# Kernel tuning notes

Hardware: AMD Instinct MI355X
Metric: run time of the kernel (lower is better)

## Reference

```python
import jax, jax.numpy as jnp
import numpy as np

B, S, D, H = 8, 1024, 1024, 16
DH = D // H


def setup_inputs() -> dict:
    key = jax.random.key(0)
    ks = jax.random.split(key, 11)
    sc = 0.02
    inp = {"inputs": jax.random.normal(ks[0], (B, S, D), dtype=jnp.float32)}
    for i, name in enumerate(["q", "k", "v", "r", "o"]):
        inp[f"W{name}"] = jax.random.normal(ks[1 + 2 * i], (D, D), dtype=jnp.float32) * sc
        inp[f"b{name}"] = jax.random.normal(ks[2 + 2 * i], (D,), dtype=jnp.float32) * sc
    return inp


def _heads(x):
    # [B, S, D] -> [B, H, S, DH]
    b, s, d = x.shape
    return x.reshape(b, s, H, DH).transpose(0, 2, 1, 3)


def reference(inputs, Wq, bq, Wk, bk, Wv, bv, Wr, br, Wo, bo):
    q = inputs @ Wq.T + bq
    k = inputs @ Wk.T + bk
    v = inputs @ Wv.T + bv
    r = inputs @ Wr.T + br
    qh, kh, vh = _heads(q), _heads(k), _heads(v)
    scores = jnp.einsum("bhsd,bhtd->bhst", qh, kh) / jnp.sqrt(jnp.float32(DH))
    attn = jax.nn.softmax(scores, axis=-1)
    # custom value transform: softmax(QK^T) @ log(sigmoid(V)), then exp
    y = jnp.exp(jnp.einsum("bhst,bhtd->bhsd", attn, jax.nn.log_sigmoid(vh)))
    # [B, H, S, DH] -> [B, S, D]
    y = y.transpose(0, 2, 1, 3).reshape(inputs.shape)
    y = r * y  # gated
    y = y @ Wo.T + bo
    return y + inputs
```

## Files before the change

kernel.cpp:

```cpp
#include <hip/hip_runtime.h>
#include <math.h>

#define Bq   8
#define Sq   1024
#define Dq   1024
#define Hq   16
#define DHq  64
#define Mq   (Bq*Sq)

typedef unsigned short u16;
typedef unsigned int   u32;
typedef __attribute__((ext_vector_type(4))) float  f4;
typedef __attribute__((ext_vector_type(4))) u16    u16x4;
typedef __attribute__((ext_vector_type(8))) __bf16 bf16x8;
typedef __attribute__((ext_vector_type(4))) float  f32x4;

#define MFMA16(acc, a, b) __builtin_amdgcn_mfma_f32_16x16x32_bf16(a, b, acc, 0, 0, 0)

__device__ __forceinline__ u16 f2b(float f) {
  u32 u = __float_as_uint(f);
  u32 r = u + 0x7FFFu + ((u >> 16) & 1u);
  return (u16)(r >> 16);
}
__device__ __forceinline__ float b2f(u16 h) {
  return __uint_as_float(((u32)h) << 16);
}
__device__ __forceinline__ float logsig(float x) {
  return fminf(x, 0.f) - log1pf(__expf(-fabsf(x)));
}
__device__ __forceinline__ void gld16(const u16* g, u16* l) {
  __builtin_amdgcn_global_load_lds(
      (const __attribute__((address_space(1))) void*)g,
      (__attribute__((address_space(3))) void*)l, 16, 0, 0);
}

__global__ __launch_bounds__(256) void cvt_kernel(const float* __restrict__ s,
                                                  u16* __restrict__ d, int n4) {
  int i = blockIdx.x * 256 + threadIdx.x;
  if (i >= n4) return;
  f4 v = *(const f4*)(s + 4 * (size_t)i);
  u32 p0 = (u32)f2b(v[0]) | ((u32)f2b(v[1]) << 16);
  u32 p1 = (u32)f2b(v[2]) | ((u32)f2b(v[3]) << 16);
  u32* dp = (u32*)(d + 4 * (size_t)i);
  dp[0] = p0; dp[1] = p1;
}

__device__ __forceinline__ void gemm_body(
    u16* As, u16* Ws_, const u16* __restrict__ A, const u16* __restrict__ W,
    const float* __restrict__ bias, const float* __restrict__ resid,
    u16* __restrict__ ob, float* __restrict__ of, int mode)
{
  char* Asc = (char*)As;
  char* Wsc = (char*)Ws_;
  const int tid = threadIdx.x;
  const int l  = tid & 63, w = tid >> 6;
  const int lo = l & 15,  lg = l >> 4;
  const int m0 = blockIdx.x * 128;
  const int n0 = blockIdx.y * 128;
  const int wr = (w >> 1) * 64;
  const int wc = (w & 1) * 64;
  const int srow = tid >> 3;
  const int scbs = ((tid & 7) * 16) ^ ((srow & 7) << 4);
  const u16* Ag = A + (size_t)(m0 + srow) * Dq + (scbs >> 1);
  const u16* Wg = W + (size_t)(n0 + srow) * Dq + (scbs >> 1);
  u16* Ad = As  + tid * 8;
  u16* Wd = Ws_ + tid * 8;

  f32x4 acc[4][4];
  #pragma unroll
  for (int i = 0; i < 4; ++i)
    #pragma unroll
    for (int j = 0; j < 4; ++j) acc[i][j] = (f32x4){0.f, 0.f, 0.f, 0.f};

  for (int k0 = 0; k0 < Dq; k0 += 64) {
    __syncthreads();
    #pragma unroll
    for (int t = 0; t < 4; ++t) {
      gld16(Ag + (size_t)t * 32 * Dq + k0, Ad + t * 32 * 64);
      gld16(Wg + (size_t)t * 32 * Dq + k0, Wd + t * 32 * 64);
    }
    __syncthreads();

    #pragma unroll
    for (int kc = 0; kc < 2; ++kc) {
      bf16x8 af[4], bfr[4];
      #pragma unroll
      for (int ff = 0; ff < 4; ++ff) {
        int ra = wr + ff * 16 + lo;
        int rb = wc + ff * 16 + lo;
        int cb = kc * 64 + lg * 16;
        af[ff]  = *(const bf16x8*)(Asc + ra * 128 + (cb ^ ((ra & 7) << 4)));
        bfr[ff] = *(const bf16x8*)(Wsc + rb * 128 + (cb ^ ((rb & 7) << 4)));
      }
      #pragma unroll
      for (int mf = 0; mf < 4; ++mf)
        #pragma unroll
        for (int nf = 0; nf < 4; ++nf)
          acc[mf][nf] = MFMA16(acc[mf][nf], af[mf], bfr[nf]);
    }
  }

  #pragma unroll
  for (int nf = 0; nf < 4; ++nf) {
    const int n = n0 + wc + nf * 16 + lo;
    const float bn = bias[n];
    if (mode == 2) {
      const int hidx = n >> 6, dh = n & 63;
      #pragma unroll
      for (int mf = 0; mf < 4; ++mf) {
        const int m = m0 + wr + mf * 16 + lg * 4;
        const int bidx = m >> 10, s = m & 1023;
        u16x4 pk;
        #pragma unroll
        for (int r = 0; r < 4; ++r) pk[r] = f2b(logsig(acc[mf][nf][r] + bn));
        *(u16x4*)(ob + ((size_t)(bidx * Hq + hidx) * DHq + dh) * Sq + s) = pk;
      }
    } else {
      #pragma unroll
      for (int mf = 0; mf < 4; ++mf) {
        #pragma unroll
        for (int r = 0; r < 4; ++r) {
          const int m = m0 + wr + mf * 16 + lg * 4 + r;
          float y = acc[mf][nf][r] + bn;
          if (mode == 0) {
            size_t a = ((size_t)((m >> 10) * Hq + (n >> 6)) * Sq + (m & 1023)) * DHq + (n & 63);
            ob[a] = f2b(y * 0.125f);
          } else if (mode == 1) {
            size_t a = ((size_t)((m >> 10) * Hq + (n >> 6)) * Sq + (m & 1023)) * DHq + (n & 63);
            ob[a] = f2b(y);
          } else if (mode == 3) {
            ob[(size_t)m * Dq + n] = f2b(y);
          } else {
            of[(size_t)m * Dq + n] = y + resid[(size_t)m * Dq + n];
          }
        }
      }
    }
  }
}

__global__ __launch_bounds__(256) void proj_kernel(
    const u16* __restrict__ Xb,
    const u16* __restrict__ Wq, const float* __restrict__ bq, u16* qh,
    const u16* __restrict__ Wk, const float* __restrict__ bk, u16* kh,
    const u16* __restrict__ Wv, const float* __restrict__ bv, u16* lsvt,
    const u16* __restrict__ Wr, const float* __restrict__ br, u16* rh)
{
  __shared__ u16 As[128 * 64];
  __shared__ u16 Ws_[128 * 64];
  const u16* W; const float* bb; u16* o; int mode = blockIdx.z;
  switch (blockIdx.z) {
    case 0:  W = Wq; bb = bq; o = qh;   break;
    case 1:  W = Wk; bb = bk; o = kh;   break;
    case 2:  W = Wv; bb = bv; o = lsvt; break;
    default: W = Wr; bb = br; o = rh;   break;
  }
  gemm_body(As, Ws_, Xb, W, bb, nullptr, o, nullptr, mode);
}

__global__ __launch_bounds__(256) void out_kernel(
    const u16* __restrict__ G, const u16* __restrict__ Wo,
    const float* __restrict__ bo, const float* __restrict__ X,
    float* __restrict__ out)
{
  __shared__ u16 As[128 * 64];
  __shared__ u16 Ws_[128 * 64];
  gemm_body(As, Ws_, G, Wo, bo, X, nullptr, out, 4);
}

__global__ __launch_bounds__(256) void attn_kernel(
    const u16* __restrict__ qh, const u16* __restrict__ kh,
    const u16* __restrict__ lsvt, const u16* __restrict__ rh,
    u16* __restrict__ g)
{
  __shared__ u16 Ks[2][64 * 64];
  __shared__ u16 Ls[2][64 * 64];
  __shared__ u16 Ps[128 * 64];
  char* Pc = (char*)Ps;

  const int tid = threadIdx.x;
  const int l  = tid & 63, w = tid >> 6;
  const int lo = l & 15,  lg = l >> 4;
  const int s0 = blockIdx.x * 128;
  const int h = blockIdx.y, b = blockIdx.z;
  const size_t hb = (size_t)(b * Hq + h) * (Sq * DHq);
  const int srow = tid >> 3;
  const int scbs = ((tid & 7) * 16) ^ ((srow & 7) << 4);

  bf16x8 qf[2][2];
  #pragma unroll
  for (int i = 0; i < 2; ++i)
    #pragma unroll
    for (int kc = 0; kc < 2; ++kc)
      qf[i][kc] = *(const bf16x8*)(qh + hb +
                    (size_t)(s0 + w * 32 + i * 16 + lo) * DHq + kc * 32 + lg * 8);

  float l_lane[2][4];
  f32x4 oacc[2][4];
  #pragma unroll
  for (int i = 0; i < 2; ++i)
    #pragma unroll
    for (int rr = 0; rr < 4; ++rr) l_lane[i][rr] = 0.f;
  #pragma unroll
  for (int i = 0; i < 2; ++i)
    #pragma unroll
    for (int f = 0; f < 4; ++f) oacc[i][f] = (f32x4){0.f, 0.f, 0.f, 0.f};

  auto stage = [&](int kt, int bb) {
    const u16* kg = kh   + hb + (size_t)(kt * 64 + srow) * DHq + (scbs >> 1);
    const u16* lg_ = lsvt + hb + (size_t)srow * Sq + kt * 64 + (scbs >> 1);
    u16* kd = (u16*)Ks[bb] + tid * 8;
    u16* ld = (u16*)Ls[bb] + tid * 8;
    gld16(kg, kd);
    gld16(kg + (size_t)32 * DHq, kd + 32 * 64);
    gld16(lg_, ld);
    gld16(lg_ + (size_t)32 * Sq, ld + 32 * 64);
  };

  stage(0, 0);
  for (int kt = 0; kt < 16; ++kt) {
    const int cur = kt & 1;
    __syncthreads();
    if (kt < 15) stage(kt + 1, cur ^ 1);
    char* Kc = (char*)Ks[cur];
    char* Lc = (char*)Ls[cur];

    f32x4 sf[2][4];
    #pragma unroll
    for (int f = 0; f < 4; ++f) {
      int rk = f * 16 + lo;
      int sw = (rk & 7) << 4;
      bf16x8 k0 = *(const bf16x8*)(Kc + rk * 128 + ((lg * 16) ^ sw));
      bf16x8 k1 = *(const bf16x8*)(Kc + rk * 128 + ((64 + lg * 16) ^ sw));
      #pragma unroll
      for (int i = 0; i < 2; ++i) {
        f32x4 s = (f32x4){0.f, 0.f, 0.f, 0.f};
        s = MFMA16(s, qf[i][0], k0);
        s = MFMA16(s, qf[i][1], k1);
        sf[i][f] = s;
      }
    }

    #pragma unroll
    for (int i = 0; i < 2; ++i) {
      const int prbase = w * 32 + i * 16 + lg * 4;
      #pragma unroll
      for (int rr = 0; rr < 4; ++rr) {
        float p0 = __expf(sf[i][0][rr]);
        float p1 = __expf(sf[i][1][rr]);
        float p2 = __expf(sf[i][2][rr]);
        float p3 = __expf(sf[i][3][rr]);
        l_lane[i][rr] += (p0 + p1) + (p2 + p3);
        const int pr = prbase + rr;
        const int sw = (pr & 7) << 4;
        *(u16*)(Pc + pr * 128 + ((lo * 2 +  0) ^ sw)) = f2b(p0);
        *(u16*)(Pc + pr * 128 + ((lo * 2 + 32) ^ sw)) = f2b(p1);
        *(u16*)(Pc + pr * 128 + ((lo * 2 + 64) ^ sw)) = f2b(p2);
        *(u16*)(Pc + pr * 128 + ((lo * 2 + 96) ^ sw)) = f2b(p3);
      }
    }
    __syncthreads();

    bf16x8 pa[2][2];
    #pragma unroll
    for (int i = 0; i < 2; ++i) {
      const int pr = w * 32 + i * 16 + lo;
      const int psw = (pr & 7) << 4;
      pa[i][0] = *(const bf16x8*)(Pc + pr * 128 + ((lg * 16) ^ psw));
      pa[i][1] = *(const bf16x8*)(Pc + pr * 128 + ((64 + lg * 16) ^ psw));
    }
    #pragma unroll
    for (int dhf = 0; dhf < 4; ++dhf) {
      const int rl = dhf * 16 + lo;
      const int lsw = (rl & 7) << 4;
      bf16x8 l0 = *(const bf16x8*)(Lc + rl * 128 + ((lg * 16) ^ lsw));
      bf16x8 l1 = *(const bf16x8*)(Lc + rl * 128 + ((64 + lg * 16) ^ lsw));
      #pragma unroll
      for (int i = 0; i < 2; ++i) {
        oacc[i][dhf] = MFMA16(oacc[i][dhf], pa[i][0], l0);
        oacc[i][dhf] = MFMA16(oacc[i][dhf], pa[i][1], l1);
      }
    }
  }

  #pragma unroll
  for (int i = 0; i < 2; ++i) {
    #pragma unroll
    for (int rr = 0; rr < 4; ++rr) {
      float lv = l_lane[i][rr];
      lv += __shfl_xor(lv, 1);
      lv += __shfl_xor(lv, 2);
      lv += __shfl_xor(lv, 4);
      lv += __shfl_xor(lv, 8);
      const float inv = 1.f / lv;
      const int srowq = s0 + w * 32 + i * 16 + lg * 4 + rr;
      const size_t rbase = ((size_t)b * Sq + srowq) * Dq + h * DHq;
      #pragma unroll
      for (int dhf = 0; dhf < 4; ++dhf) {
        const int col = dhf * 16 + lo;
        float y = __expf(oacc[i][dhf][rr] * inv);
        g[rbase + col] = f2b(y * b2f(rh[rbase + col]));
      }
    }
  }
}

extern "C" void kernel_launch(void* const* d_in, const int* in_sizes, int n_in,
                              void* d_out, int out_size, void* d_ws, size_t ws_size,
                              hipStream_t stream)
{
  const float* X  = (const float*)d_in[0];
  const float* Wq = (const float*)d_in[1];  const float* bq = (const float*)d_in[2];
  const float* Wk = (const float*)d_in[3];  const float* bk = (const float*)d_in[4];
  const float* Wv = (const float*)d_in[5];  const float* bv = (const float*)d_in[6];
  const float* Wr = (const float*)d_in[7];  const float* br = (const float*)d_in[8];
  const float* Wo = (const float*)d_in[9];  const float* bo = (const float*)d_in[10];
  float* out = (float*)d_out;

  const size_t NX = (size_t)Mq * Dq;
  const size_t NW = (size_t)Dq * Dq;
  u16* Xb   = (u16*)d_ws;
  u16* Wqb  = Xb   + NX;
  u16* Wkb  = Wqb  + NW;
  u16* Wvb  = Wkb  + NW;
  u16* Wrb  = Wvb  + NW;
  u16* Wob  = Wrb  + NW;
  u16* qhb  = Wob  + NW;
  u16* khb  = qhb  + NX;
  u16* lsvt = khb  + NX;
  u16* rhb  = lsvt + NX;
  u16* gb   = rhb  + NX;

  dim3 blk(256);
  hipLaunchKernelGGL(cvt_kernel, dim3(NX / 1024), blk, 0, stream, X,  Xb,  (int)(NX / 4));
  hipLaunchKernelGGL(cvt_kernel, dim3(NW / 1024), blk, 0, stream, Wq, Wqb, (int)(NW / 4));
  hipLaunchKernelGGL(cvt_kernel, dim3(NW / 1024), blk, 0, stream, Wk, Wkb, (int)(NW / 4));
  hipLaunchKernelGGL(cvt_kernel, dim3(NW / 1024), blk, 0, stream, Wv, Wvb, (int)(NW / 4));
  hipLaunchKernelGGL(cvt_kernel, dim3(NW / 1024), blk, 0, stream, Wr, Wrb, (int)(NW / 4));
  hipLaunchKernelGGL(cvt_kernel, dim3(NW / 1024), blk, 0, stream, Wo, Wob, (int)(NW / 4));

  hipLaunchKernelGGL(proj_kernel, dim3(Mq / 128, Dq / 128, 4), blk, 0, stream,
                     Xb, Wqb, bq, qhb, Wkb, bk, khb, Wvb, bv, lsvt, Wrb, br, rhb);

  hipLaunchKernelGGL(attn_kernel, dim3(Sq / 128, Hq, Bq), blk, 0, stream,
                     qhb, khb, lsvt, rhb, gb);

  hipLaunchKernelGGL(out_kernel, dim3(Mq / 128, Dq / 128), blk, 0, stream,
                     gb, Wob, bo, X, out);
}
```

Baseline: 331.6 us.

## Double-buffer GEMM tiles, fuse conversions, and remap blocks for XCD locality

Merges the six fp32-to-bf16 conversion launches into one kernel. Double-buffers the GEMM K-loop in LDS so the next tile's loads overlap the current tile's MFMAs, with one barrier per step. Remaps the flat block index in the projection and attention kernels so blocks sharing a weight slice or head land on the same XCD, for better L2 reuse. Doubled LDS per block may lower occupancy.

```diff
diff --git a/kernel.cpp b/kernel.cpp
--- a/kernel.cpp
+++ b/kernel.cpp
@@ -34,37 +34,52 @@
       (__attribute__((address_space(3))) void*)l, 16, 0, 0);
 }
 
-__global__ __launch_bounds__(256) void cvt_kernel(const float* __restrict__ s,
-                                                  u16* __restrict__ d, int n4) {
-  int i = blockIdx.x * 256 + threadIdx.x;
-  if (i >= n4) return;
-  f4 v = *(const f4*)(s + 4 * (size_t)i);
+#define NX4c (Mq*Dq/4)
+#define NW4c (Dq*Dq/4)
+__global__ __launch_bounds__(256) void cvt_all_kernel(
+    const float* __restrict__ X,  const float* __restrict__ Wq,
+    const float* __restrict__ Wk, const float* __restrict__ Wv,
+    const float* __restrict__ Wr, const float* __restrict__ Wo,
+    u16* Xb, u16* Wqb, u16* Wkb, u16* Wvb, u16* Wrb, u16* Wob)
+{
+  int id = blockIdx.x * 256 + threadIdx.x;
+  if (id >= NX4c + 5 * NW4c) return;
+  const float* s; u16* d; int off;
+  if (id < NX4c) { s = X; d = Xb; off = id; }
+  else {
+    int r = id - NX4c;
+    int w = r >> 18;
+    off = r & (NW4c - 1);
+    switch (w) {
+      case 0:  s = Wq; d = Wqb; break;
+      case 1:  s = Wk; d = Wkb; break;
+      case 2:  s = Wv; d = Wvb; break;
+      case 3:  s = Wr; d = Wrb; break;
+      default: s = Wo; d = Wob; break;
+    }
+  }
+  f4 v = *(const f4*)(s + 4 * (size_t)off);
   u32 p0 = (u32)f2b(v[0]) | ((u32)f2b(v[1]) << 16);
   u32 p1 = (u32)f2b(v[2]) | ((u32)f2b(v[3]) << 16);
-  u32* dp = (u32*)(d + 4 * (size_t)i);
+  u32* dp = (u32*)(d + 4 * (size_t)off);
   dp[0] = p0; dp[1] = p1;
 }
 
 __device__ __forceinline__ void gemm_body(
-    u16* As, u16* Ws_, const u16* __restrict__ A, const u16* __restrict__ W,
+    u16* As, u16* Ws_, int m0, int n0,
+    const u16* __restrict__ A, const u16* __restrict__ W,
     const float* __restrict__ bias, const float* __restrict__ resid,
     u16* __restrict__ ob, float* __restrict__ of, int mode)
 {
-  char* Asc = (char*)As;
-  char* Wsc = (char*)Ws_;
   const int tid = threadIdx.x;
   const int l  = tid & 63, w = tid >> 6;
   const int lo = l & 15,  lg = l >> 4;
-  const int m0 = blockIdx.x * 128;
-  const int n0 = blockIdx.y * 128;
   const int wr = (w >> 1) * 64;
   const int wc = (w & 1) * 64;
   const int srow = tid >> 3;
   const int scbs = ((tid & 7) * 16) ^ ((srow & 7) << 4);
   const u16* Ag = A + (size_t)(m0 + srow) * Dq + (scbs >> 1);
   const u16* Wg = W + (size_t)(n0 + srow) * Dq + (scbs >> 1);
-  u16* Ad = As  + tid * 8;
-  u16* Wd = Ws_ + tid * 8;
 
   f32x4 acc[4][4];
   #pragma unroll
@@ -72,15 +87,31 @@
     #pragma unroll
     for (int j = 0; j < 4; ++j) acc[i][j] = (f32x4){0.f, 0.f, 0.f, 0.f};
 
-  for (int k0 = 0; k0 < Dq; k0 += 64) {
-    __syncthreads();
+  {
+    u16* Ad = As  + tid * 8;
+    u16* Wd = Ws_ + tid * 8;
     #pragma unroll
     for (int t = 0; t < 4; ++t) {
-      gld16(Ag + (size_t)t * 32 * Dq + k0, Ad + t * 32 * 64);
-      gld16(Wg + (size_t)t * 32 * Dq + k0, Wd + t * 32 * 64);
-    }
-    __syncthreads();
-
+      gld16(Ag + (size_t)t * 32 * Dq, Ad + t * 32 * 64);
+      gld16(Wg + (size_t)t * 32 * Dq, Wd + t * 32 * 64);
+    }
+  }
+  __syncthreads();
+
+  for (int ks = 0; ks < 16; ++ks) {
+    const int cur = ks & 1;
+    if (ks < 15) {
+      const int k0 = (ks + 1) * 64;
+      u16* Ad = As  + (cur ^ 1) * 8192 + tid * 8;
+      u16* Wd = Ws_ + (cur ^ 1) * 8192 + tid * 8;
+      #pragma unroll
+      for (int t = 0; t < 4; ++t) {
+        gld16(Ag + (size_t)t * 32 * Dq + k0, Ad + t * 32 * 64);
+        gld16(Wg + (size_t)t * 32 * Dq + k0, Wd + t * 32 * 64);
+      }
+    }
+    char* Asc = (char*)(As  + cur * 8192);
+    char* Wsc = (char*)(Ws_ + cur * 8192);
     #pragma unroll
     for (int kc = 0; kc < 2; ++kc) {
       bf16x8 af[4], bfr[4];
@@ -98,6 +129,7 @@
         for (int nf = 0; nf < 4; ++nf)
           acc[mf][nf] = MFMA16(acc[mf][nf], af[mf], bfr[nf]);
     }
+    __syncthreads();
   }
 
   #pragma unroll
@@ -146,16 +178,22 @@
     const u16* __restrict__ Wv, const float* __restrict__ bv, u16* lsvt,
     const u16* __restrict__ Wr, const float* __restrict__ br, u16* rh)
 {
-  __shared__ u16 As[128 * 64];
-  __shared__ u16 Ws_[128 * 64];
-  const u16* W; const float* bb; u16* o; int mode = blockIdx.z;
-  switch (blockIdx.z) {
-    case 0:  W = Wq; bb = bq; o = qh;   break;
-    case 1:  W = Wk; bb = bk; o = kh;   break;
-    case 2:  W = Wv; bb = bv; o = lsvt; break;
-    default: W = Wr; bb = br; o = rh;   break;
-  }
-  gemm_body(As, Ws_, Xb, W, bb, nullptr, o, nullptr, mode);
+  __shared__ u16 As[2 * 128 * 64];
+  __shared__ u16 Ws_[2 * 128 * 64];
+  const int n = blockIdx.x;
+  const int xcd = n & 7;
+  const int slot = n >> 3;
+  const int g = xcd * 4 + (slot >> 6);
+  const int x = slot & 63;
+  const int y = g & 7, z = g >> 3;
+  const u16* W; const float* bb; u16* o; int mode;
+  switch (z) {
+    case 0:  W = Wq; bb = bq; o = qh;   mode = 0; break;
+    case 1:  W = Wk; bb = bk; o = kh;   mode = 1; break;
+    case 2:  W = Wv; bb = bv; o = lsvt; mode = 2; break;
+    default: W = Wr; bb = br; o = rh;   mode = 3; break;
+  }
+  gemm_body(As, Ws_, x * 128, y * 128, Xb, W, bb, nullptr, o, nullptr, mode);
 }
 
 __global__ __launch_bounds__(256) void out_kernel(
@@ -163,9 +201,11 @@
     const float* __restrict__ bo, const float* __restrict__ X,
     float* __restrict__ out)
 {
-  __shared__ u16 As[128 * 64];
-  __shared__ u16 Ws_[128 * 64];
-  gemm_body(As, Ws_, G, Wo, bo, X, nullptr, out, 4);
+  __shared__ u16 As[2 * 128 * 64];
+  __shared__ u16 Ws_[2 * 128 * 64];
+  const int n = blockIdx.x;
+  const int y = n & 7, x = n >> 3;
+  gemm_body(As, Ws_, x * 128, y * 128, G, Wo, bo, X, nullptr, out, 4);
 }
 
 __global__ __launch_bounds__(256) void attn_kernel(
@@ -181,8 +221,14 @@
   const int tid = threadIdx.x;
   const int l  = tid & 63, w = tid >> 6;
   const int lo = l & 15,  lg = l >> 4;
-  const int s0 = blockIdx.x * 128;
-  const int h = blockIdx.y, b = blockIdx.z;
+  const int nblk = blockIdx.x;
+  const int xcd = nblk & 7;
+  const int m_ = nblk >> 3;
+  const int gi = m_ >> 3;
+  const int x  = m_ & 7;
+  const int grp = xcd * 16 + gi;
+  const int h = grp & 15, b = grp >> 4;
+  const int s0 = x * 128;
   const size_t hb = (size_t)(b * Hq + h) * (Sq * DHq);
   const int srow = tid >> 3;
   const int scbs = ((tid & 7) * 16) ^ ((srow & 7) << 4);
@@ -206,11 +252,11 @@
     #pragma unroll
     for (int f = 0; f < 4; ++f) oacc[i][f] = (f32x4){0.f, 0.f, 0.f, 0.f};
 
-  auto stage = [&](int kt, int bb) {
-    const u16* kg = kh   + hb + (size_t)(kt * 64 + srow) * DHq + (scbs >> 1);
+  auto stage = [&](int kt, int buf) {
+    const u16* kg  = kh   + hb + (size_t)(kt * 64 + srow) * DHq + (scbs >> 1);
     const u16* lg_ = lsvt + hb + (size_t)srow * Sq + kt * 64 + (scbs >> 1);
-    u16* kd = (u16*)Ks[bb] + tid * 8;
-    u16* ld = (u16*)Ls[bb] + tid * 8;
+    u16* kd = (u16*)Ks[buf] + tid * 8;
+    u16* ld = (u16*)Ls[buf] + tid * 8;
     gld16(kg, kd);
     gld16(kg + (size_t)32 * DHq, kd + 32 * 64);
     gld16(lg_, ld);
@@ -332,19 +378,16 @@
   u16* gb   = rhb  + NX;
 
   dim3 blk(256);
-  hipLaunchKernelGGL(cvt_kernel, dim3(NX / 1024), blk, 0, stream, X,  Xb,  (int)(NX / 4));
-  hipLaunchKernelGGL(cvt_kernel, dim3(NW / 1024), blk, 0, stream, Wq, Wqb, (int)(NW / 4));
-  hipLaunchKernelGGL(cvt_kernel, dim3(NW / 1024), blk, 0, stream, Wk, Wkb, (int)(NW / 4));
-  hipLaunchKernelGGL(cvt_kernel, dim3(NW / 1024), blk, 0, stream, Wv, Wvb, (int)(NW / 4));
-  hipLaunchKernelGGL(cvt_kernel, dim3(NW / 1024), blk, 0, stream, Wr, Wrb, (int)(NW / 4));
-  hipLaunchKernelGGL(cvt_kernel, dim3(NW / 1024), blk, 0, stream, Wo, Wob, (int)(NW / 4));
-
-  hipLaunchKernelGGL(proj_kernel, dim3(Mq / 128, Dq / 128, 4), blk, 0, stream,
+  const int ncvt = (NX4c + 5 * NW4c + 255) / 256;
+  hipLaunchKernelGGL(cvt_all_kernel, dim3(ncvt), blk, 0, stream,
+                     X, Wq, Wk, Wv, Wr, Wo, Xb, Wqb, Wkb, Wvb, Wrb, Wob);
+
+  hipLaunchKernelGGL(proj_kernel, dim3(2048), blk, 0, stream,
                      Xb, Wqb, bq, qhb, Wkb, bk, khb, Wvb, bv, lsvt, Wrb, br, rhb);
 
-  hipLaunchKernelGGL(attn_kernel, dim3(Sq / 128, Hq, Bq), blk, 0, stream,
+  hipLaunchKernelGGL(attn_kernel, dim3(1024), blk, 0, stream,
                      qhb, khb, lsvt, rhb, gb);
 
-  hipLaunchKernelGGL(out_kernel, dim3(Mq / 128, Dq / 128), blk, 0, stream,
+  hipLaunchKernelGGL(out_kernel, dim3(512), blk, 0, stream,
                      gb, Wob, bo, X, out);
 }
```

New measurement: 359.1 us. 1.08x slower.
